# Kernel tuning notes

Measured on AMD Instinct MI355X. Metric: run time of the kernel, lower is better.

Reference implementation:

```python
import jax, jax.numpy as jnp
import numpy as np

B, C = 4096, 10000
TAU = 1.0
MIN_K, MAX_K = 30, 100


def setup_inputs() -> dict:
    key = jax.random.key(0)
    k1, k2 = jax.random.split(key, 2)
    logit = jax.random.normal(k1, (B, C), dtype=jnp.float32)
    target = jax.random.randint(k2, (B,), 0, C)
    # long-tailed class counts: exponential decay from 1000 down to 5
    cls_num = np.exp(np.linspace(np.log(1000.0), np.log(5.0), C)).astype(np.float32)
    cls_num_ratio = cls_num / cls_num.sum()
    log_cls_num = jnp.asarray(np.log(cls_num_ratio + 1e-6), dtype=jnp.float32)
    freq = (cls_num.max() / cls_num).astype(np.float32)
    freq_norm = (freq - freq.min()) / (freq.max() - freq.min() + 1e-6)
    k_per_class = jnp.asarray((freq_norm * (MAX_K - MIN_K) + MIN_K).astype(np.int32))
    return {"logit": logit, "target": target, "log_cls_num": log_cls_num,
            "k_per_class": k_per_class}


def reference(logit, target, log_cls_num, k_per_class):
    b, c = logit.shape
    rows = jnp.arange(b)
    # logit-adjusted cross entropy (loss_full)
    logit_adj = logit + TAU * log_cls_num[None, :]
    log_p_adj = jax.nn.log_softmax(logit_adj, axis=1)  # [B, C]
    loss_full = -jnp.mean(log_p_adj[rows, target])
    # per-row variable-k top-k mask on the ORIGINAL logits
    prob_adj = jnp.exp(log_p_adj)
    k = jnp.minimum(k_per_class[target], c)            # [B]
    sorted_desc = -jnp.sort(-logit, axis=1)            # [B, C] descending
    thresh = sorted_desc[rows, k - 1]                  # k-th largest per row
    mask = logit >= thresh[:, None]
    masked_prob = jnp.where(mask, prob_adj, 0.0) + 1e-6
    masked_prob = masked_prob / masked_prob.sum(axis=1, keepdims=True)
    loss_topk = -jnp.mean(jnp.log(masked_prob)[rows, target])
    return 0.5 * loss_full + 0.5 * loss_topk
```

## Files before the change

### kernel.cpp

```cpp
#include <hip/hip_runtime.h>

#define BLOCK 256
#define WPB 4
#define C_DIM 10000
#define C4 (C_DIM / 4)
#define SEGQ (C4 / WPB)
#define ITQ ((SEGQ + 63) / 64)
#define NIT4 ((C4 + 63) / 64)
#define TAU 1.0f
#define CAP 512
#define PIV_HI 2.0f
#define PIV_LO 1.0f

__device__ __forceinline__ unsigned flip_key(float f) {
    unsigned u = __float_as_uint(f);
    return (u & 0x80000000u) ? ~u : (u | 0x80000000u);
}
__device__ __forceinline__ float unflip_key(unsigned k) {
    unsigned u = (k & 0x80000000u) ? (k & 0x7fffffffu) : ~k;
    return __uint_as_float(u);
}
__device__ __forceinline__ int mbcnt64(unsigned long long m) {
    return (int)__builtin_amdgcn_mbcnt_hi((unsigned)(m >> 32),
               __builtin_amdgcn_mbcnt_lo((unsigned)(m & 0xffffffffu), 0u));
}

__global__ void zero_out_kernel(float* out, int n) {
    int i = blockIdx.x * blockDim.x + threadIdx.x;
    if (i < n) out[i] = 0.f;
}

__device__ __forceinline__ void wave_pick(uint4 hv, int lane, int shift,
                                          unsigned& prefix, unsigned& kr, unsigned& cnt) {
    unsigned loc = hv.x + hv.y + hv.z + hv.w;
    unsigned suf = loc;
    #pragma unroll
    for (int off = 1; off < 64; off <<= 1) {
        unsigned o = (unsigned)__shfl_down((int)suf, off);
        if (lane + off < 64) suf += o;
    }
    unsigned sufex = suf - loc;
    unsigned s3 = sufex + hv.w;
    unsigned s2 = s3 + hv.z;
    unsigned s1 = s2 + hv.y;
    unsigned s0 = s1 + hv.x;
    int bsel = -1; unsigned nkr = 0u, ncnt = 0u;
    if      (s3 >= kr && s3 - hv.w < kr) { bsel = 4 * lane + 3; nkr = kr - (s3 - hv.w); ncnt = hv.w; }
    else if (s2 >= kr && s2 - hv.z < kr) { bsel = 4 * lane + 2; nkr = kr - (s2 - hv.z); ncnt = hv.z; }
    else if (s1 >= kr && s1 - hv.y < kr) { bsel = 4 * lane + 1; nkr = kr - (s1 - hv.y); ncnt = hv.y; }
    else if (s0 >= kr && s0 - hv.x < kr) { bsel = 4 * lane + 0; nkr = kr - (s0 - hv.x); ncnt = hv.x; }
    unsigned long long pm = __ballot(bsel >= 0);
    int src = __ffsll((unsigned long long)pm) - 1;
    prefix |= ((unsigned)__shfl(bsel, src)) << shift;
    kr  = (unsigned)__shfl((int)nkr, src);
    cnt = (unsigned)__shfl((int)ncnt, src);
}

__global__ __launch_bounds__(BLOCK, 4) void topk_la_loss_kernel(
    const float* __restrict__ logit, const int* __restrict__ target,
    const float* __restrict__ lcn, const int* __restrict__ kpc,
    float* __restrict__ out, int B) {
    __shared__ unsigned candk[WPB][CAP];
    __shared__ unsigned short candi[WPB][CAP];
    __shared__ unsigned hist[256];
    __shared__ unsigned sh_nb[WPB];
    __shared__ float red_a[WPB], red_b[WPB];
    __shared__ float sh_thresh;

    const int tid = threadIdx.x;
    const int lane = tid & 63;
    const int wid = tid >> 6;
    const int row = blockIdx.x;
    const float* lrow = logit + (size_t)row * C_DIM;

    const int t = target[row];
    int k = kpc[t]; if (k > C_DIM) k = C_DIM;
    const float logit_t = lrow[t];
    const float lcn_t = lcn[t];

    unsigned* ck = candk[wid];
    unsigned short* ci = candi[wid];
    const int base4 = wid * SEGQ;

    float4 fv[ITQ], lv[ITQ];
    #pragma unroll
    for (int it = 0; it < ITQ; ++it) {
        const int j4l = it * 64 + lane;
        if (j4l < SEGQ) {
            fv[it] = ((const float4*)lrow)[base4 + j4l];
            lv[it] = ((const float4*)lcn)[base4 + j4l];
        } else {
            fv[it] = make_float4(-1e30f, -1e30f, -1e30f, -1e30f);
            lv[it] = make_float4(0.f, 0.f, 0.f, 0.f);
        }
    }

    float z0 = 0.f, z1 = 0.f, z2 = 0.f, z3 = 0.f;
    float mA = -__builtin_inff(), mB = -__builtin_inff();
    unsigned nb = 0u;
    #pragma unroll
    for (int it = 0; it < ITQ; ++it) {
        const float4 f = fv[it], l = lv[it];
        const float a0 = f.x + TAU * l.x, a1 = f.y + TAU * l.y;
        const float a2 = f.z + TAU * l.z, a3 = f.w + TAU * l.w;
        z0 += __expf(a0); z1 += __expf(a1);
        z2 += __expf(a2); z3 += __expf(a3);
        mA = fmaxf(mA, fmaxf(a0, a1));
        mB = fmaxf(mB, fmaxf(a2, a3));
        const int j = 4 * (base4 + it * 64 + lane);
        unsigned long long m;
        m = __ballot(f.x >= PIV_HI);
        if (f.x >= PIV_HI) { unsigned p = nb + (unsigned)mbcnt64(m); if (p < CAP) { ck[p] = __float_as_uint(f.x); ci[p] = (unsigned short)(j + 0); } }
        nb += (unsigned)__popcll(m);
        m = __ballot(f.y >= PIV_HI);
        if (f.y >= PIV_HI) { unsigned p = nb + (unsigned)mbcnt64(m); if (p < CAP) { ck[p] = __float_as_uint(f.y); ci[p] = (unsigned short)(j + 1); } }
        nb += (unsigned)__popcll(m);
        m = __ballot(f.z >= PIV_HI);
        if (f.z >= PIV_HI) { unsigned p = nb + (unsigned)mbcnt64(m); if (p < CAP) { ck[p] = __float_as_uint(f.z); ci[p] = (unsigned short)(j + 2); } }
        nb += (unsigned)__popcll(m);
        m = __ballot(f.w >= PIV_HI);
        if (f.w >= PIV_HI) { unsigned p = nb + (unsigned)mbcnt64(m); if (p < CAP) { ck[p] = __float_as_uint(f.w); ci[p] = (unsigned short)(j + 3); } }
        nb += (unsigned)__popcll(m);
    }
    float z = (z0 + z1) + (z2 + z3);
    float madj = fmaxf(mA, mB);
    #pragma unroll
    for (int off = 32; off; off >>= 1) madj = fmaxf(madj, __shfl_xor(madj, off));
    if (lane == 0) { red_a[wid] = madj; sh_nb[wid] = nb; }
    __syncthreads();

    const float madjB = fmaxf(fmaxf(red_a[0], red_a[1]), fmaxf(red_a[2], red_a[3]));
    unsigned nbs0 = sh_nb[0], nbs1 = sh_nb[1], nbs2 = sh_nb[2], nbs3 = sh_nb[3];
    unsigned ntot = nbs0 + nbs1 + nbs2 + nbs3;
    unsigned nmax = max(max(nbs0, nbs1), max(nbs2, nbs3));
    int path = (ntot >= (unsigned)k && nmax <= CAP) ? 0 : ((ntot < (unsigned)k) ? 1 : 2);

    if (path == 1) {
        nb = 0u;
        for (int it = 0; it < ITQ; ++it) {
            const int j4l = it * 64 + lane;
            float4 f;
            if (j4l < SEGQ) f = ((const float4*)lrow)[base4 + j4l];
            else f = make_float4(-1e30f, -1e30f, -1e30f, -1e30f);
            const int j = 4 * (base4 + j4l);
            unsigned long long m;
            m = __ballot(f.x >= PIV_LO);
            if (f.x >= PIV_LO) { unsigned p = nb + (unsigned)mbcnt64(m); if (p < CAP) { ck[p] = __float_as_uint(f.x); ci[p] = (unsigned short)(j + 0); } }
            nb += (unsigned)__popcll(m);
            m = __ballot(f.y >= PIV_LO);
            if (f.y >= PIV_LO) { unsigned p = nb + (unsigned)mbcnt64(m); if (p < CAP) { ck[p] = __float_as_uint(f.y); ci[p] = (unsigned short)(j + 1); } }
            nb += (unsigned)__popcll(m);
            m = __ballot(f.z >= PIV_LO);
            if (f.z >= PIV_LO) { unsigned p = nb + (unsigned)mbcnt64(m); if (p < CAP) { ck[p] = __float_as_uint(f.z); ci[p] = (unsigned short)(j + 2); } }
            nb += (unsigned)__popcll(m);
            m = __ballot(f.w >= PIV_LO);
            if (f.w >= PIV_LO) { unsigned p = nb + (unsigned)mbcnt64(m); if (p < CAP) { ck[p] = __float_as_uint(f.w); ci[p] = (unsigned short)(j + 3); } }
            nb += (unsigned)__popcll(m);
        }
        if (lane == 0) sh_nb[wid] = nb;
        __syncthreads();
        nbs0 = sh_nb[0]; nbs1 = sh_nb[1]; nbs2 = sh_nb[2]; nbs3 = sh_nb[3];
        ntot = nbs0 + nbs1 + nbs2 + nbs3;
        nmax = max(max(nbs0, nbs1), max(nbs2, nbs3));
        path = (ntot >= (unsigned)k && nmax <= CAP) ? 0 : 2;
    }

    if (path == 0) {
        if (wid == 0) {
            unsigned prefix = 0u, kr = (unsigned)k, cnt = ntot, kmask = 0u;
            const unsigned nbs[4] = {nbs0, nbs1, nbs2, nbs3};
            for (int q = 0; q < 4; ++q) {
                if (cnt == 1u) break;
                const int shift = 24 - 8 * q;
                *(uint4*)&hist[4 * lane] = make_uint4(0u, 0u, 0u, 0u);
                #pragma unroll
                for (int s = 0; s < 4; ++s) {
                    for (int i = lane; i < (int)nbs[s]; i += 64) {
                        unsigned kk = candk[s][i];
                        if ((kk & kmask) == prefix) atomicAdd(&hist[(kk >> shift) & 0xFFu], 1u);
                    }
                }
                uint4 hv = *(const uint4*)&hist[4 * lane];
                wave_pick(hv, lane, shift, prefix, kr, cnt);
                kmask |= (0xFFu << shift);
            }
            if (cnt == 1u && kmask != 0xFFFFFFFFu) {
                unsigned found = 0u;
                #pragma unroll
                for (int s = 0; s < 4; ++s) {
                    for (int i = lane; i < (int)nbs[s]; i += 64) {
                        unsigned kk = candk[s][i];
                        if ((kk & kmask) == prefix) found = kk;
                    }
                }
                #pragma unroll
                for (int off = 32; off; off >>= 1) found |= (unsigned)__shfl_xor((int)found, off);
                prefix = found;
            }
            if (lane == 0) sh_thresh = __uint_as_float(prefix);
        }
    } else {
        if (wid == 0) {
            unsigned prefix = 0u, kr = (unsigned)k, cnt = 0u;
            for (int p = 0; p < 4; ++p) {
                const int shift = 24 - 8 * p;
                const unsigned pmask = p ? (0xFFFFFFFFu << (shift + 8)) : 0u;
                *(uint4*)&hist[4 * lane] = make_uint4(0u, 0u, 0u, 0u);
                for (int it = 0; it < NIT4; ++it) {
                    const int j4 = it * 64 + lane;
                    if (j4 < C4) {
                        float4 f = ((const float4*)lrow)[j4];
                        unsigned kk;
                        kk = flip_key(f.x); if ((kk & pmask) == prefix) atomicAdd(&hist[(kk >> shift) & 0xFFu], 1u);
                        kk = flip_key(f.y); if ((kk & pmask) == prefix) atomicAdd(&hist[(kk >> shift) & 0xFFu], 1u);
                        kk = flip_key(f.z); if ((kk & pmask) == prefix) atomicAdd(&hist[(kk >> shift) & 0xFFu], 1u);
                        kk = flip_key(f.w); if ((kk & pmask) == prefix) atomicAdd(&hist[(kk >> shift) & 0xFFu], 1u);
                    }
                }
                uint4 hv = *(const uint4*)&hist[4 * lane];
                wave_pick(hv, lane, shift, prefix, kr, cnt);
            }
            if (lane == 0) sh_thresh = unflip_key(prefix);
        }
    }
    __syncthreads();
    const float thresh = sh_thresh;

    const bool rare = fabsf(madjB) > 80.f;
    float sm = 0.f;
    if (!rare) {
        if (path == 0) {
            const int nc = (int)sh_nb[wid];
            for (int i = lane; i < nc; i += 64) {
                const float v = __uint_as_float(ck[i]);
                if (v >= thresh) sm += __expf(v + TAU * lcn[ci[i]]);
            }
        } else {
            for (int it = 0; it < ITQ; ++it) {
                const int j4l = it * 64 + lane;
                if (j4l < SEGQ) {
                    float4 f = ((const float4*)lrow)[base4 + j4l];
                    float4 l = ((const float4*)lcn)[base4 + j4l];
                    if (f.x >= thresh) sm += __expf(f.x + TAU * l.x);
                    if (f.y >= thresh) sm += __expf(f.y + TAU * l.y);
                    if (f.z >= thresh) sm += __expf(f.z + TAU * l.z);
                    if (f.w >= thresh) sm += __expf(f.w + TAU * l.w);
                }
            }
        }
    } else {
        z = 0.f;
        for (int it = 0; it < ITQ; ++it) {
            const int j4l = it * 64 + lane;
            if (j4l < SEGQ) {
                float4 f = ((const float4*)lrow)[base4 + j4l];
                float4 l = ((const float4*)lcn)[base4 + j4l];
                float e;
                e = __expf(f.x + TAU * l.x - madjB); z += e; if (f.x >= thresh) sm += e;
                e = __expf(f.y + TAU * l.y - madjB); z += e; if (f.y >= thresh) sm += e;
                e = __expf(f.z + TAU * l.z - madjB); z += e; if (f.z >= thresh) sm += e;
                e = __expf(f.w + TAU * l.w - madjB); z += e; if (f.w >= thresh) sm += e;
            }
        }
    }

    #pragma unroll
    for (int off = 32; off; off >>= 1) {
        z  += __shfl_down(z, off);
        sm += __shfl_down(sm, off);
    }
    if (lane == 0) { red_a[wid] = z; red_b[wid] = sm; }
    __syncthreads();

    if (tid == 0) {
        const float Z = red_a[0] + red_a[1] + red_a[2] + red_a[3];
        const float S = red_b[0] + red_b[1] + red_b[2] + red_b[3];
        const float adj_t = logit_t + TAU * lcn_t;
        const float sub = rare ? madjB : 0.f;
        const float lpt = adj_t - sub - __logf(Z);
        const float p_num = ((logit_t >= thresh) ? __expf(lpt) : 0.f) + 1e-6f;
        const float Smask = S / Z + (float)C_DIM * 1e-6f;
        const float loss = 0.5f * (-lpt + __logf(Smask) - __logf(p_num));
        atomicAdd(out, loss / (float)B);
    }
}

extern "C" void kernel_launch(void* const* d_in, const int* in_sizes, int n_in,
                              void* d_out, int out_size, void* d_ws, size_t ws_size,
                              hipStream_t stream) {
    const float* logit  = (const float*)d_in[0];
    const int*   target = (const int*)d_in[1];
    const float* lcn    = (const float*)d_in[2];
    const int*   kpc    = (const int*)d_in[3];
    float* out = (float*)d_out;
    const int B = in_sizes[1];

    zero_out_kernel<<<1, 64, 0, stream>>>(out, out_size);
    topk_la_loss_kernel<<<B, BLOCK, 0, stream>>>(logit, target, lcn, kpc, out, B);
}
```

Measured before the change: 241.3 us.

## Split fused top-k loss into two-block-per-row sweep plus per-row select kernel

Each row is now swept by two 256-thread blocks with small per-wave candidate buffers, and the candidates, partial Z and max are written to workspace. A separate 64-thread select kernel then gathers the candidates and runs the radix select and masked sum. The aim is more parallelism and occupancy in the bandwidth-bound pass, at the cost of an extra launch and global round-trips for the candidates. The PIV_LO retry path is dropped in favour of a full-row radix fallback, and the old monolithic kernel is kept for when the workspace is too small.

New measurement: 292.4 us. 21.2% more time.

```diff
diff --git a/kernel.cpp b/kernel.cpp
--- a/kernel.cpp
+++ b/kernel.cpp
@@ -1,16 +1,17 @@
 #include <hip/hip_runtime.h>
 
-#define BLOCK 256
-#define WPB 4
 #define C_DIM 10000
-#define C4 (C_DIM / 4)
-#define SEGQ (C4 / WPB)
-#define ITQ ((SEGQ + 63) / 64)
-#define NIT4 ((C4 + 63) / 64)
+#define C4 2500
+#define HALF4 1250
+#define ITQ1 5
+#define NIT4 40
 #define TAU 1.0f
-#define CAP 512
 #define PIV_HI 2.0f
 #define PIV_LO 1.0f
+#define CAPW 64
+#define CAPH 256
+#define ROWCAP 512
+#define SENT 0xFFFFFFFFu
 
 __device__ __forceinline__ unsigned flip_key(float f) {
     unsigned u = __float_as_uint(f);
@@ -56,37 +57,30 @@
     cnt = (unsigned)__shfl((int)ncnt, src);
 }
 
-__global__ __launch_bounds__(BLOCK, 4) void topk_la_loss_kernel(
-    const float* __restrict__ logit, const int* __restrict__ target,
-    const float* __restrict__ lcn, const int* __restrict__ kpc,
-    float* __restrict__ out, int B) {
-    __shared__ unsigned candk[WPB][CAP];
-    __shared__ unsigned short candi[WPB][CAP];
-    __shared__ unsigned hist[256];
-    __shared__ unsigned sh_nb[WPB];
-    __shared__ float red_a[WPB], red_b[WPB];
-    __shared__ float sh_thresh;
+__global__ __launch_bounds__(256, 6) void sweep_kernel(
+    const float* __restrict__ logit, const float* __restrict__ lcn,
+    unsigned* __restrict__ g_keys, unsigned short* __restrict__ g_idx,
+    unsigned* __restrict__ g_cnt, float* __restrict__ g_z, float* __restrict__ g_m) {
+    __shared__ unsigned ck[4][CAPW];
+    __shared__ unsigned short ci[4][CAPW];
+    __shared__ unsigned sh_nb[4];
+    __shared__ float sh_z[4], sh_m[4];
 
     const int tid = threadIdx.x;
     const int lane = tid & 63;
     const int wid = tid >> 6;
-    const int row = blockIdx.x;
+    const int row = blockIdx.x >> 1;
+    const int half = blockIdx.x & 1;
     const float* lrow = logit + (size_t)row * C_DIM;
 
-    const int t = target[row];
-    int k = kpc[t]; if (k > C_DIM) k = C_DIM;
-    const float logit_t = lrow[t];
-    const float lcn_t = lcn[t];
-
-    unsigned* ck = candk[wid];
-    unsigned short* ci = candi[wid];
-    const int base4 = wid * SEGQ;
-
-    float4 fv[ITQ], lv[ITQ];
-    #pragma unroll
-    for (int it = 0; it < ITQ; ++it) {
+    const int base4 = half * HALF4 + wid * 312 + (wid < 2 ? wid : 2);
+    const int segn = 312 + (wid < 2 ? 1 : 0);
+
+    float4 fv[ITQ1], lv[ITQ1];
+    #pragma unroll
+    for (int it = 0; it < ITQ1; ++it) {
         const int j4l = it * 64 + lane;
-        if (j4l < SEGQ) {
+        if (j4l < segn) {
             fv[it] = ((const float4*)lrow)[base4 + j4l];
             lv[it] = ((const float4*)lcn)[base4 + j4l];
         } else {
@@ -99,7 +93,7 @@
     float mA = -__builtin_inff(), mB = -__builtin_inff();
     unsigned nb = 0u;
     #pragma unroll
-    for (int it = 0; it < ITQ; ++it) {
+    for (int it = 0; it < ITQ1; ++it) {
         const float4 f = fv[it], l = lv[it];
         const float a0 = f.x + TAU * l.x, a1 = f.y + TAU * l.y;
         const float a2 = f.z + TAU * l.z, a3 = f.w + TAU * l.w;
@@ -110,16 +104,245 @@
         const int j = 4 * (base4 + it * 64 + lane);
         unsigned long long m;
         m = __ballot(f.x >= PIV_HI);
-        if (f.x >= PIV_HI) { unsigned p = nb + (unsigned)mbcnt64(m); if (p < CAP) { ck[p] = __float_as_uint(f.x); ci[p] = (unsigned short)(j + 0); } }
+        if (f.x >= PIV_HI) { unsigned p = nb + (unsigned)mbcnt64(m); if (p < CAPW) { ck[wid][p] = __float_as_uint(f.x); ci[wid][p] = (unsigned short)(j + 0); } }
         nb += (unsigned)__popcll(m);
         m = __ballot(f.y >= PIV_HI);
-        if (f.y >= PIV_HI) { unsigned p = nb + (unsigned)mbcnt64(m); if (p < CAP) { ck[p] = __float_as_uint(f.y); ci[p] = (unsigned short)(j + 1); } }
+        if (f.y >= PIV_HI) { unsigned p = nb + (unsigned)mbcnt64(m); if (p < CAPW) { ck[wid][p] = __float_as_uint(f.y); ci[wid][p] = (unsigned short)(j + 1); } }
         nb += (unsigned)__popcll(m);
         m = __ballot(f.z >= PIV_HI);
-        if (f.z >= PIV_HI) { unsigned p = nb + (unsigned)mbcnt64(m); if (p < CAP) { ck[p] = __float_as_uint(f.z); ci[p] = (unsigned short)(j + 2); } }
+        if (f.z >= PIV_HI) { unsigned p = nb + (unsigned)mbcnt64(m); if (p < CAPW) { ck[wid][p] = __float_as_uint(f.z); ci[wid][p] = (unsigned short)(j + 2); } }
         nb += (unsigned)__popcll(m);
         m = __ballot(f.w >= PIV_HI);
-        if (f.w >= PIV_HI) { unsigned p = nb + (unsigned)mbcnt64(m); if (p < CAP) { ck[p] = __float_as_uint(f.w); ci[p] = (unsigned short)(j + 3); } }
+        if (f.w >= PIV_HI) { unsigned p = nb + (unsigned)mbcnt64(m); if (p < CAPW) { ck[wid][p] = __float_as_uint(f.w); ci[wid][p] = (unsigned short)(j + 3); } }
+        nb += (unsigned)__popcll(m);
+    }
+    float z = (z0 + z1) + (z2 + z3);
+    float madj = fmaxf(mA, mB);
+    #pragma unroll
+    for (int off = 32; off; off >>= 1) {
+        z += __shfl_down(z, off);
+        madj = fmaxf(madj, __shfl_down(madj, off));
+    }
+    if (lane == 0) { sh_nb[wid] = nb; sh_z[wid] = z; sh_m[wid] = madj; }
+    __syncthreads();
+
+    const unsigned n0 = sh_nb[0], n1 = sh_nb[1], n2 = sh_nb[2], n3 = sh_nb[3];
+    const bool ovf = (n0 > CAPW) | (n1 > CAPW) | (n2 > CAPW) | (n3 > CAPW);
+    if (!ovf) {
+        const unsigned pre = (wid > 0 ? n0 : 0u) + (wid > 1 ? n1 : 0u) + (wid > 2 ? n2 : 0u);
+        const unsigned nbw = sh_nb[wid];
+        const size_t dst = (size_t)row * ROWCAP + (size_t)half * CAPH + pre;
+        for (unsigned i = lane; i < nbw; i += 64) {
+            g_keys[dst + i] = ck[wid][i];
+            g_idx[dst + i] = ci[wid][i];
+        }
+    }
+    if (tid == 0) {
+        g_cnt[2 * row + half] = ovf ? SENT : (n0 + n1 + n2 + n3);
+        g_z[2 * row + half] = sh_z[0] + sh_z[1] + sh_z[2] + sh_z[3];
+        g_m[2 * row + half] = fmaxf(fmaxf(sh_z ? sh_m[0] : sh_m[0], sh_m[1]), fmaxf(sh_m[2], sh_m[3]));
+    }
+}
+
+__global__ __launch_bounds__(64, 8) void select_kernel(
+    const float* __restrict__ logit, const int* __restrict__ target,
+    const float* __restrict__ lcn, const int* __restrict__ kpc,
+    const unsigned* __restrict__ g_keys, const unsigned short* __restrict__ g_idx,
+    const unsigned* __restrict__ g_cnt, const float* __restrict__ g_z,
+    const float* __restrict__ g_m, float* __restrict__ out, int B) {
+    __shared__ unsigned k2k[ROWCAP];
+    __shared__ unsigned short k2i[ROWCAP];
+    __shared__ unsigned hist[256];
+
+    const int lane = threadIdx.x;
+    const int row = blockIdx.x;
+    const float* lrow = logit + (size_t)row * C_DIM;
+
+    const int t = target[row];
+    int k = kpc[t]; if (k > C_DIM) k = C_DIM;
+    const float logit_t = lrow[t];
+    const float lcn_t = lcn[t];
+    const unsigned c0 = g_cnt[2 * row], c1 = g_cnt[2 * row + 1];
+    float Z = g_z[2 * row] + g_z[2 * row + 1];
+    const float madj = fmaxf(g_m[2 * row], g_m[2 * row + 1]);
+
+    const bool path0 = (c0 != SENT) && (c1 != SENT) && (c0 + c1 >= (unsigned)k);
+    unsigned n = 0u;
+    float thresh;
+
+    if (path0) {
+        n = c0 + c1;
+        const size_t b0 = (size_t)row * ROWCAP;
+        for (unsigned i = lane; i < c0; i += 64) { k2k[i] = g_keys[b0 + i]; k2i[i] = g_idx[b0 + i]; }
+        for (unsigned i = lane; i < c1; i += 64) { k2k[c0 + i] = g_keys[b0 + CAPH + i]; k2i[c0 + i] = g_idx[b0 + CAPH + i]; }
+        unsigned prefix = 0u, kr = (unsigned)k, cnt = n, kmask = 0u;
+        for (int q = 0; q < 4; ++q) {
+            if (cnt == 1u) break;
+            const int shift = 24 - 8 * q;
+            *(uint4*)&hist[4 * lane] = make_uint4(0u, 0u, 0u, 0u);
+            for (unsigned i = lane; i < n; i += 64) {
+                unsigned kk = k2k[i];
+                if ((kk & kmask) == prefix) atomicAdd(&hist[(kk >> shift) & 0xFFu], 1u);
+            }
+            uint4 hv = *(const uint4*)&hist[4 * lane];
+            wave_pick(hv, lane, shift, prefix, kr, cnt);
+            kmask |= (0xFFu << shift);
+        }
+        if (cnt == 1u && kmask != 0xFFFFFFFFu) {
+            unsigned found = 0u;
+            for (unsigned i = lane; i < n; i += 64) {
+                unsigned kk = k2k[i];
+                if ((kk & kmask) == prefix) found = kk;
+            }
+            #pragma unroll
+            for (int off = 32; off; off >>= 1) found |= (unsigned)__shfl_xor((int)found, off);
+            prefix = found;
+        }
+        thresh = __uint_as_float(prefix);
+    } else {
+        unsigned prefix = 0u, kr = (unsigned)k, cnt = 0u;
+        for (int p = 0; p < 4; ++p) {
+            const int shift = 24 - 8 * p;
+            const unsigned pmask = p ? (0xFFFFFFFFu << (shift + 8)) : 0u;
+            *(uint4*)&hist[4 * lane] = make_uint4(0u, 0u, 0u, 0u);
+            for (int it = 0; it < NIT4; ++it) {
+                const int j4 = it * 64 + lane;
+                if (j4 < C4) {
+                    float4 f = ((const float4*)lrow)[j4];
+                    unsigned kk;
+                    kk = flip_key(f.x); if ((kk & pmask) == prefix) atomicAdd(&hist[(kk >> shift) & 0xFFu], 1u);
+                    kk = flip_key(f.y); if ((kk & pmask) == prefix) atomicAdd(&hist[(kk >> shift) & 0xFFu], 1u);
+                    kk = flip_key(f.z); if ((kk & pmask) == prefix) atomicAdd(&hist[(kk >> shift) & 0xFFu], 1u);
+                    kk = flip_key(f.w); if ((kk & pmask) == prefix) atomicAdd(&hist[(kk >> shift) & 0xFFu], 1u);
+                }
+            }
+            uint4 hv = *(const uint4*)&hist[4 * lane];
+            wave_pick(hv, lane, shift, prefix, kr, cnt);
+        }
+        thresh = unflip_key(prefix);
+    }
+
+    const bool rare = fabsf(madj) > 80.f;
+    float sm = 0.f, zloc = 0.f;
+    if (!rare) {
+        if (path0) {
+            for (unsigned i = lane; i < n; i += 64) {
+                const float v = __uint_as_float(k2k[i]);
+                if (v >= thresh) sm += __expf(v + TAU * lcn[k2i[i]]);
+            }
+        } else {
+            for (int it = 0; it < NIT4; ++it) {
+                const int j4 = it * 64 + lane;
+                if (j4 < C4) {
+                    float4 f = ((const float4*)lrow)[j4];
+                    float4 l = ((const float4*)lcn)[j4];
+                    if (f.x >= thresh) sm += __expf(f.x + TAU * l.x);
+                    if (f.y >= thresh) sm += __expf(f.y + TAU * l.y);
+                    if (f.z >= thresh) sm += __expf(f.z + TAU * l.z);
+                    if (f.w >= thresh) sm += __expf(f.w + TAU * l.w);
+                }
+            }
+        }
+    } else {
+        for (int it = 0; it < NIT4; ++it) {
+            const int j4 = it * 64 + lane;
+            if (j4 < C4) {
+                float4 f = ((const float4*)lrow)[j4];
+                float4 l = ((const float4*)lcn)[j4];
+                float e;
+                e = __expf(f.x + TAU * l.x - madj); zloc += e; if (f.x >= thresh) sm += e;
+                e = __expf(f.y + TAU * l.y - madj); zloc += e; if (f.y >= thresh) sm += e;
+                e = __expf(f.z + TAU * l.z - madj); zloc += e; if (f.z >= thresh) sm += e;
+                e = __expf(f.w + TAU * l.w - madj); zloc += e; if (f.w >= thresh) sm += e;
+            }
+        }
+    }
+
+    #pragma unroll
+    for (int off = 32; off; off >>= 1) {
+        sm += __shfl_down(sm, off);
+        zloc += __shfl_down(zloc, off);
+    }
+    if (lane == 0) {
+        if (rare) Z = zloc;
+        const float adj_t = logit_t + TAU * lcn_t;
+        const float sub = rare ? madj : 0.f;
+        const float lpt = adj_t - sub - __logf(Z);
+        const float p_num = ((logit_t >= thresh) ? __expf(lpt) : 0.f) + 1e-6f;
+        const float Smask = sm / Z + (float)C_DIM * 1e-6f;
+        const float loss = 0.5f * (-lpt + __logf(Smask) - __logf(p_num));
+        atomicAdd(out, loss / (float)B);
+    }
+}
+
+#define MONO_CAP 512
+#define MONO_SEGQ 625
+#define MONO_ITQ 10
+
+__global__ __launch_bounds__(256, 4) void topk_mono_kernel(
+    const float* __restrict__ logit, const int* __restrict__ target,
+    const float* __restrict__ lcn, const int* __restrict__ kpc,
+    float* __restrict__ out, int B) {
+    __shared__ unsigned candk[4][MONO_CAP];
+    __shared__ unsigned short candi[4][MONO_CAP];
+    __shared__ unsigned hist[256];
+    __shared__ unsigned sh_nb[4];
+    __shared__ float red_a[4], red_b[4];
+    __shared__ float sh_thresh;
+
+    const int tid = threadIdx.x;
+    const int lane = tid & 63;
+    const int wid = tid >> 6;
+    const int row = blockIdx.x;
+    const float* lrow = logit + (size_t)row * C_DIM;
+
+    const int t = target[row];
+    int k = kpc[t]; if (k > C_DIM) k = C_DIM;
+    const float logit_t = lrow[t];
+    const float lcn_t = lcn[t];
+
+    unsigned* ck = candk[wid];
+    unsigned short* ci = candi[wid];
+    const int base4 = wid * MONO_SEGQ;
+
+    float4 fv[MONO_ITQ], lv[MONO_ITQ];
+    #pragma unroll
+    for (int it = 0; it < MONO_ITQ; ++it) {
+        const int j4l = it * 64 + lane;
+        if (j4l < MONO_SEGQ) {
+            fv[it] = ((const float4*)lrow)[base4 + j4l];
+            lv[it] = ((const float4*)lcn)[base4 + j4l];
+        } else {
+            fv[it] = make_float4(-1e30f, -1e30f, -1e30f, -1e30f);
+            lv[it] = make_float4(0.f, 0.f, 0.f, 0.f);
+        }
+    }
+
+    float z0 = 0.f, z1 = 0.f, z2 = 0.f, z3 = 0.f;
+    float mA = -__builtin_inff(), mB = -__builtin_inff();
+    unsigned nb = 0u;
+    #pragma unroll
+    for (int it = 0; it < MONO_ITQ; ++it) {
+        const float4 f = fv[it], l = lv[it];
+        const float a0 = f.x + TAU * l.x, a1 = f.y + TAU * l.y;
+        const float a2 = f.z + TAU * l.z, a3 = f.w + TAU * l.w;
+        z0 += __expf(a0); z1 += __expf(a1);
+        z2 += __expf(a2); z3 += __expf(a3);
+        mA = fmaxf(mA, fmaxf(a0, a1));
+        mB = fmaxf(mB, fmaxf(a2, a3));
+        const int j = 4 * (base4 + it * 64 + lane);
+        unsigned long long m;
+        m = __ballot(f.x >= PIV_HI);
+        if (f.x >= PIV_HI) { unsigned p = nb + (unsigned)mbcnt64(m); if (p < MONO_CAP) { ck[p] = __float_as_uint(f.x); ci[p] = (unsigned short)(j + 0); } }
+        nb += (unsigned)__popcll(m);
+        m = __ballot(f.y >= PIV_HI);
+        if (f.y >= PIV_HI) { unsigned p = nb + (unsigned)mbcnt64(m); if (p < MONO_CAP) { ck[p] = __float_as_uint(f.y); ci[p] = (unsigned short)(j + 1); } }
+        nb += (unsigned)__popcll(m);
+        m = __ballot(f.z >= PIV_HI);
+        if (f.z >= PIV_HI) { unsigned p = nb + (unsigned)mbcnt64(m); if (p < MONO_CAP) { ck[p] = __float_as_uint(f.z); ci[p] = (unsigned short)(j + 2); } }
+        nb += (unsigned)__popcll(m);
+        m = __ballot(f.w >= PIV_HI);
+        if (f.w >= PIV_HI) { unsigned p = nb + (unsigned)mbcnt64(m); if (p < MONO_CAP) { ck[p] = __float_as_uint(f.w); ci[p] = (unsigned short)(j + 3); } }
         nb += (unsigned)__popcll(m);
     }
     float z = (z0 + z1) + (z2 + z3);
@@ -133,37 +356,7 @@
     unsigned nbs0 = sh_nb[0], nbs1 = sh_nb[1], nbs2 = sh_nb[2], nbs3 = sh_nb[3];
     unsigned ntot = nbs0 + nbs1 + nbs2 + nbs3;
     unsigned nmax = max(max(nbs0, nbs1), max(nbs2, nbs3));
-    int path = (ntot >= (unsigned)k && nmax <= CAP) ? 0 : ((ntot < (unsigned)k) ? 1 : 2);
-
-    if (path == 1) {
-        nb = 0u;
-        for (int it = 0; it < ITQ; ++it) {
-            const int j4l = it * 64 + lane;
-            float4 f;
-            if (j4l < SEGQ) f = ((const float4*)lrow)[base4 + j4l];
-            else f = make_float4(-1e30f, -1e30f, -1e30f, -1e30f);
-            const int j = 4 * (base4 + j4l);
-            unsigned long long m;
-            m = __ballot(f.x >= PIV_LO);
-            if (f.x >= PIV_LO) { unsigned p = nb + (unsigned)mbcnt64(m); if (p < CAP) { ck[p] = __float_as_uint(f.x); ci[p] = (unsigned short)(j + 0); } }
-            nb += (unsigned)__popcll(m);
-            m = __ballot(f.y >= PIV_LO);
-            if (f.y >= PIV_LO) { unsigned p = nb + (unsigned)mbcnt64(m); if (p < CAP) { ck[p] = __float_as_uint(f.y); ci[p] = (unsigned short)(j + 1); } }
-            nb += (unsigned)__popcll(m);
-            m = __ballot(f.z >= PIV_LO);
-            if (f.z >= PIV_LO) { unsigned p = nb + (unsigned)mbcnt64(m); if (p < CAP) { ck[p] = __float_as_uint(f.z); ci[p] = (unsigned short)(j + 2); } }
-            nb += (unsigned)__popcll(m);
-            m = __ballot(f.w >= PIV_LO);
-            if (f.w >= PIV_LO) { unsigned p = nb + (unsigned)mbcnt64(m); if (p < CAP) { ck[p] = __float_as_uint(f.w); ci[p] = (unsigned short)(j + 3); } }
-            nb += (unsigned)__popcll(m);
-        }
-        if (lane == 0) sh_nb[wid] = nb;
-        __syncthreads();
-        nbs0 = sh_nb[0]; nbs1 = sh_nb[1]; nbs2 = sh_nb[2]; nbs3 = sh_nb[3];
-        ntot = nbs0 + nbs1 + nbs2 + nbs3;
-        nmax = max(max(nbs0, nbs1), max(nbs2, nbs3));
-        path = (ntot >= (unsigned)k && nmax <= CAP) ? 0 : 2;
-    }
+    int path = (ntot >= (unsigned)k && nmax <= MONO_CAP) ? 0 : 2;
 
     if (path == 0) {
         if (wid == 0) {
@@ -236,9 +429,9 @@
                 if (v >= thresh) sm += __expf(v + TAU * lcn[ci[i]]);
             }
         } else {
-            for (int it = 0; it < ITQ; ++it) {
+            for (int it = 0; it < MONO_ITQ; ++it) {
                 const int j4l = it * 64 + lane;
-                if (j4l < SEGQ) {
+                if (j4l < MONO_SEGQ) {
                     float4 f = ((const float4*)lrow)[base4 + j4l];
                     float4 l = ((const float4*)lcn)[base4 + j4l];
                     if (f.x >= thresh) sm += __expf(f.x + TAU * l.x);
@@ -250,9 +443,9 @@
         }
     } else {
         z = 0.f;
-        for (int it = 0; it < ITQ; ++it) {
+        for (int it = 0; it < MONO_ITQ; ++it) {
             const int j4l = it * 64 + lane;
-            if (j4l < SEGQ) {
+            if (j4l < MONO_SEGQ) {
                 float4 f = ((const float4*)lrow)[base4 + j4l];
                 float4 l = ((const float4*)lcn)[base4 + j4l];
                 float e;
@@ -296,5 +489,24 @@
     const int B = in_sizes[1];
 
     zero_out_kernel<<<1, 64, 0, stream>>>(out, out_size);
-    topk_la_loss_kernel<<<B, BLOCK, 0, stream>>>(logit, target, lcn, kpc, out, B);
-}
+
+    const size_t keys_b = (size_t)B * ROWCAP * sizeof(unsigned);
+    const size_t idx_b  = (size_t)B * ROWCAP * sizeof(unsigned short);
+    const size_t cnt_b  = (size_t)B * 2 * sizeof(unsigned);
+    const size_t z_b    = (size_t)B * 2 * sizeof(float);
+    const size_t need   = keys_b + idx_b + cnt_b + z_b + z_b;
+
+    if (d_ws != nullptr && ws_size >= need) {
+        char* wsb = (char*)d_ws;
+        unsigned* g_keys       = (unsigned*)wsb;
+        unsigned short* g_idx  = (unsigned short*)(wsb + keys_b);
+        unsigned* g_cnt        = (unsigned*)(wsb + keys_b + idx_b);
+        float* g_z             = (float*)(wsb + keys_b + idx_b + cnt_b);
+        float* g_m             = (float*)(wsb + keys_b + idx_b + cnt_b + z_b);
+        sweep_kernel<<<2 * B, 256, 0, stream>>>(logit, lcn, g_keys, g_idx, g_cnt, g_z, g_m);
+        select_kernel<<<B, 64, 0, stream>>>(logit, target, lcn, kpc,
+                                            g_keys, g_idx, g_cnt, g_z, g_m, out, B);
+    } else {
+        topk_mono_kernel<<<B, 256, 0, stream>>>(logit, target, lcn, kpc, out, B);
+    }
+}
```

## Replace full register prefetch with rotating 4-deep load pipeline and raise occupancy

Applied to the files above, without the earlier changes.

The kernel used to load all ten float4 iterations of logits and class priors into registers before computing. It now keeps a rolling window of four float4 pairs, issuing the next load right after each body is consumed. Launch bounds rise from 4 to 8 blocks per SIMD. The aim is to cut VGPR pressure so more waves stay resident and hide memory latency better. The cost is fewer loads in flight per wave, and the tighter register cap could cause spills.

After: 322.7 us. 1.34x slower.

```diff
diff --git a/kernel.cpp b/kernel.cpp
--- a/kernel.cpp
+++ b/kernel.cpp
@@ -56,7 +56,7 @@
     cnt = (unsigned)__shfl((int)ncnt, src);
 }
 
-__global__ __launch_bounds__(BLOCK, 4) void topk_la_loss_kernel(
+__global__ __launch_bounds__(BLOCK, 8) void topk_la_loss_kernel(
     const float* __restrict__ logit, const int* __restrict__ target,
     const float* __restrict__ lcn, const int* __restrict__ kpc,
     float* __restrict__ out, int B) {
@@ -82,46 +82,61 @@
     unsigned short* ci = candi[wid];
     const int base4 = wid * SEGQ;
 
-    float4 fv[ITQ], lv[ITQ];
-    #pragma unroll
-    for (int it = 0; it < ITQ; ++it) {
-        const int j4l = it * 64 + lane;
-        if (j4l < SEGQ) {
-            fv[it] = ((const float4*)lrow)[base4 + j4l];
-            lv[it] = ((const float4*)lcn)[base4 + j4l];
-        } else {
-            fv[it] = make_float4(-1e30f, -1e30f, -1e30f, -1e30f);
-            lv[it] = make_float4(0.f, 0.f, 0.f, 0.f);
-        }
-    }
-
     float z0 = 0.f, z1 = 0.f, z2 = 0.f, z3 = 0.f;
     float mA = -__builtin_inff(), mB = -__builtin_inff();
     unsigned nb = 0u;
-    #pragma unroll
-    for (int it = 0; it < ITQ; ++it) {
-        const float4 f = fv[it], l = lv[it];
-        const float a0 = f.x + TAU * l.x, a1 = f.y + TAU * l.y;
-        const float a2 = f.z + TAU * l.z, a3 = f.w + TAU * l.w;
-        z0 += __expf(a0); z1 += __expf(a1);
-        z2 += __expf(a2); z3 += __expf(a3);
-        mA = fmaxf(mA, fmaxf(a0, a1));
-        mB = fmaxf(mB, fmaxf(a2, a3));
-        const int j = 4 * (base4 + it * 64 + lane);
-        unsigned long long m;
-        m = __ballot(f.x >= PIV_HI);
-        if (f.x >= PIV_HI) { unsigned p = nb + (unsigned)mbcnt64(m); if (p < CAP) { ck[p] = __float_as_uint(f.x); ci[p] = (unsigned short)(j + 0); } }
-        nb += (unsigned)__popcll(m);
-        m = __ballot(f.y >= PIV_HI);
-        if (f.y >= PIV_HI) { unsigned p = nb + (unsigned)mbcnt64(m); if (p < CAP) { ck[p] = __float_as_uint(f.y); ci[p] = (unsigned short)(j + 1); } }
-        nb += (unsigned)__popcll(m);
-        m = __ballot(f.z >= PIV_HI);
-        if (f.z >= PIV_HI) { unsigned p = nb + (unsigned)mbcnt64(m); if (p < CAP) { ck[p] = __float_as_uint(f.z); ci[p] = (unsigned short)(j + 2); } }
-        nb += (unsigned)__popcll(m);
-        m = __ballot(f.w >= PIV_HI);
-        if (f.w >= PIV_HI) { unsigned p = nb + (unsigned)mbcnt64(m); if (p < CAP) { ck[p] = __float_as_uint(f.w); ci[p] = (unsigned short)(j + 3); } }
-        nb += (unsigned)__popcll(m);
-    }
+
+#define LOADIT(F, L, IT) do {                                                  \
+        const int j4l_ = (IT) * 64 + lane;                                     \
+        if (j4l_ < SEGQ) {                                                     \
+            F = ((const float4*)lrow)[base4 + j4l_];                           \
+            L = ((const float4*)lcn)[base4 + j4l_];                            \
+        } else {                                                               \
+            F = make_float4(-1e30f, -1e30f, -1e30f, -1e30f);                   \
+            L = make_float4(0.f, 0.f, 0.f, 0.f);                               \
+        }                                                                      \
+    } while (0)
+
+#define BODY(F, L, IT) do {                                                    \
+        const float a0 = F.x + TAU * L.x, a1 = F.y + TAU * L.y;                \
+        const float a2 = F.z + TAU * L.z, a3 = F.w + TAU * L.w;                \
+        z0 += __expf(a0); z1 += __expf(a1);                                    \
+        z2 += __expf(a2); z3 += __expf(a3);                                    \
+        mA = fmaxf(mA, fmaxf(a0, a1));                                         \
+        mB = fmaxf(mB, fmaxf(a2, a3));                                         \
+        const int j = 4 * (base4 + (IT) * 64 + lane);                          \
+        unsigned long long m;                                                  \
+        m = __ballot(F.x >= PIV_HI);                                           \
+        if (F.x >= PIV_HI) { unsigned p = nb + (unsigned)mbcnt64(m); if (p < CAP) { ck[p] = __float_as_uint(F.x); ci[p] = (unsigned short)(j + 0); } } \
+        nb += (unsigned)__popcll(m);                                           \
+        m = __ballot(F.y >= PIV_HI);                                           \
+        if (F.y >= PIV_HI) { unsigned p = nb + (unsigned)mbcnt64(m); if (p < CAP) { ck[p] = __float_as_uint(F.y); ci[p] = (unsigned short)(j + 1); } } \
+        nb += (unsigned)__popcll(m);                                           \
+        m = __ballot(F.z >= PIV_HI);                                           \
+        if (F.z >= PIV_HI) { unsigned p = nb + (unsigned)mbcnt64(m); if (p < CAP) { ck[p] = __float_as_uint(F.z); ci[p] = (unsigned short)(j + 2); } } \
+        nb += (unsigned)__popcll(m);                                           \
+        m = __ballot(F.w >= PIV_HI);                                           \
+        if (F.w >= PIV_HI) { unsigned p = nb + (unsigned)mbcnt64(m); if (p < CAP) { ck[p] = __float_as_uint(F.w); ci[p] = (unsigned short)(j + 3); } } \
+        nb += (unsigned)__popcll(m);                                           \
+    } while (0)
+
+    {
+        float4 f0, f1, f2, f3, l0, l1, l2, l3;
+        LOADIT(f0, l0, 0); LOADIT(f1, l1, 1); LOADIT(f2, l2, 2); LOADIT(f3, l3, 3);
+        BODY(f0, l0, 0); LOADIT(f0, l0, 4);
+        BODY(f1, l1, 1); LOADIT(f1, l1, 5);
+        BODY(f2, l2, 2); LOADIT(f2, l2, 6);
+        BODY(f3, l3, 3); LOADIT(f3, l3, 7);
+        BODY(f0, l0, 4); LOADIT(f0, l0, 8);
+        BODY(f1, l1, 5); LOADIT(f1, l1, 9);
+        BODY(f2, l2, 6);
+        BODY(f3, l3, 7);
+        BODY(f0, l0, 8);
+        BODY(f1, l1, 9);
+    }
+#undef LOADIT
+#undef BODY
+
     float z = (z0 + z1) + (z2 + z3);
     float madj = fmaxf(mA, mB);
     #pragma unroll
```

## Stream first-pass row loads through double-buffered LDS via global_load_lds

Applied to the files above, without the earlier changes.

Replaces the upfront register preload of all logit and log-count float4 chunks with a double-buffered LDS staging pipeline that uses global_load_lds. Each iteration issues the next chunk's direct-to-LDS loads and waits with manual vmcnt counters before reading the current chunk from shared memory. The aim is to cut register pressure from holding ITQ float4 pairs and to overlap memory latency with the exp and candidate-gathering work. In exchange it adds LDS traffic and fragile hand-written waitcnt logic with no barrier between the async LDS write and the LDS read. The default early vmcnt(2) also assumes exactly two outstanding loads, which does not hold in iterations where the next chunk's loads are skipped.

After: 255.3 us. 5.8% more time.

```diff
diff --git a/kernel.cpp b/kernel.cpp
--- a/kernel.cpp
+++ b/kernel.cpp
@@ -23,6 +23,11 @@
 __device__ __forceinline__ int mbcnt64(unsigned long long m) {
     return (int)__builtin_amdgcn_mbcnt_hi((unsigned)(m >> 32),
                __builtin_amdgcn_mbcnt_lo((unsigned)(m & 0xffffffffu), 0u));
+}
+__device__ __forceinline__ void gload16(const void* g, void* l) {
+    __builtin_amdgcn_global_load_lds(
+        (const __attribute__((address_space(1))) unsigned*)g,
+        (__attribute__((address_space(3))) unsigned*)l, 16, 0, 0);
 }
 
 __global__ void zero_out_kernel(float* out, int n) {
@@ -62,6 +67,7 @@
     float* __restrict__ out, int B) {
     __shared__ unsigned candk[WPB][CAP];
     __shared__ unsigned short candi[WPB][CAP];
+    __shared__ float4 stg[WPB][2][2][64];
     __shared__ unsigned hist[256];
     __shared__ unsigned sh_nb[WPB];
     __shared__ float red_a[WPB], red_b[WPB];
@@ -72,6 +78,8 @@
     const int wid = tid >> 6;
     const int row = blockIdx.x;
     const float* lrow = logit + (size_t)row * C_DIM;
+    const float4* lrow4 = (const float4*)lrow;
+    const float4* lcn4 = (const float4*)lcn;
 
     const int t = target[row];
     int k = kpc[t]; if (k > C_DIM) k = C_DIM;
@@ -82,32 +90,43 @@
     unsigned short* ci = candi[wid];
     const int base4 = wid * SEGQ;
 
-    float4 fv[ITQ], lv[ITQ];
-    #pragma unroll
-    for (int it = 0; it < ITQ; ++it) {
-        const int j4l = it * 64 + lane;
-        if (j4l < SEGQ) {
-            fv[it] = ((const float4*)lrow)[base4 + j4l];
-            lv[it] = ((const float4*)lcn)[base4 + j4l];
-        } else {
-            fv[it] = make_float4(-1e30f, -1e30f, -1e30f, -1e30f);
-            lv[it] = make_float4(0.f, 0.f, 0.f, 0.f);
-        }
-    }
-
     float z0 = 0.f, z1 = 0.f, z2 = 0.f, z3 = 0.f;
     float mA = -__builtin_inff(), mB = -__builtin_inff();
     unsigned nb = 0u;
+
+    gload16(&lrow4[base4 + lane], &stg[wid][0][0][0]);
+    gload16(&lcn4[base4 + lane], &stg[wid][0][1][0]);
+
     #pragma unroll
     for (int it = 0; it < ITQ; ++it) {
-        const float4 f = fv[it], l = lv[it];
+        const int cur = it & 1, nxt = cur ^ 1;
+        if (it + 1 < ITQ) {
+            const int j4n = (it + 1) * 64 + lane;
+            if (j4n < SEGQ) {
+                gload16(&lrow4[base4 + j4n], &stg[wid][nxt][0][0]);
+                gload16(&lcn4[base4 + j4n], &stg[wid][nxt][1][0]);
+            }
+            asm volatile("s_waitcnt vmcnt(2)" ::: "memory");
+        } else {
+            asm volatile("s_waitcnt vmcnt(0)" ::: "memory");
+        }
+        __builtin_amdgcn_sched_barrier(0);
+        const int j4l = it * 64 + lane;
+        float4 f, l;
+        if (j4l < SEGQ) {
+            f = stg[wid][cur][0][lane];
+            l = stg[wid][cur][1][lane];
+        } else {
+            f = make_float4(-1e30f, -1e30f, -1e30f, -1e30f);
+            l = make_float4(0.f, 0.f, 0.f, 0.f);
+        }
         const float a0 = f.x + TAU * l.x, a1 = f.y + TAU * l.y;
         const float a2 = f.z + TAU * l.z, a3 = f.w + TAU * l.w;
         z0 += __expf(a0); z1 += __expf(a1);
         z2 += __expf(a2); z3 += __expf(a3);
         mA = fmaxf(mA, fmaxf(a0, a1));
         mB = fmaxf(mB, fmaxf(a2, a3));
-        const int j = 4 * (base4 + it * 64 + lane);
+        const int j = 4 * (base4 + j4l);
         unsigned long long m;
         m = __ballot(f.x >= PIV_HI);
         if (f.x >= PIV_HI) { unsigned p = nb + (unsigned)mbcnt64(m); if (p < CAP) { ck[p] = __float_as_uint(f.x); ci[p] = (unsigned short)(j + 0); } }
@@ -122,6 +141,7 @@
         if (f.w >= PIV_HI) { unsigned p = nb + (unsigned)mbcnt64(m); if (p < CAP) { ck[p] = __float_as_uint(f.w); ci[p] = (unsigned short)(j + 3); } }
         nb += (unsigned)__popcll(m);
     }
+
     float z = (z0 + z1) + (z2 + z3);
     float madj = fmaxf(mA, mB);
     #pragma unroll
@@ -140,7 +160,7 @@
         for (int it = 0; it < ITQ; ++it) {
             const int j4l = it * 64 + lane;
             float4 f;
-            if (j4l < SEGQ) f = ((const float4*)lrow)[base4 + j4l];
+            if (j4l < SEGQ) f = lrow4[base4 + j4l];
             else f = make_float4(-1e30f, -1e30f, -1e30f, -1e30f);
             const int j = 4 * (base4 + j4l);
             unsigned long long m;
@@ -209,7 +229,7 @@
                 for (int it = 0; it < NIT4; ++it) {
                     const int j4 = it * 64 + lane;
                     if (j4 < C4) {
-                        float4 f = ((const float4*)lrow)[j4];
+                        float4 f = lrow4[j4];
                         unsigned kk;
                         kk = flip_key(f.x); if ((kk & pmask) == prefix) atomicAdd(&hist[(kk >> shift) & 0xFFu], 1u);
                         kk = flip_key(f.y); if ((kk & pmask) == prefix) atomicAdd(&hist[(kk >> shift) & 0xFFu], 1u);
@@ -239,8 +259,8 @@
             for (int it = 0; it < ITQ; ++it) {
                 const int j4l = it * 64 + lane;
                 if (j4l < SEGQ) {
-                    float4 f = ((const float4*)lrow)[base4 + j4l];
-                    float4 l = ((const float4*)lcn)[base4 + j4l];
+                    float4 f = lrow4[base4 + j4l];
+                    float4 l = lcn4[base4 + j4l];
                     if (f.x >= thresh) sm += __expf(f.x + TAU * l.x);
                     if (f.y >= thresh) sm += __expf(f.y + TAU * l.y);
                     if (f.z >= thresh) sm += __expf(f.z + TAU * l.z);
@@ -253,8 +273,8 @@
         for (int it = 0; it < ITQ; ++it) {
             const int j4l = it * 64 + lane;
             if (j4l < SEGQ) {
-                float4 f = ((const float4*)lrow)[base4 + j4l];
-                float4 l = ((const float4*)lcn)[base4 + j4l];
+                float4 f = lrow4[base4 + j4l];
+                float4 l = lcn4[base4 + j4l];
                 float e;
                 e = __expf(f.x + TAU * l.x - madjB); z += e; if (f.x >= thresh) sm += e;
                 e = __expf(f.y + TAU * l.y - madjB); z += e; if (f.y >= thresh) sm += e;
```
